# Kernel optimization log

Hardware: AMD Instinct MI355X
Metric: run time of the kernel (lower is better)

Reference implementation:

```python
import jax, jax.numpy as jnp
import numpy as np

EMBED_DIM = 1024
N_HEADS = 16
HEAD_DIM = EMBED_DIM // N_HEADS
BATCH = 2
SEQ = 2048


def setup_inputs() -> dict:
    key = jax.random.key(0)
    ks = jax.random.split(key, 12)
    s = 1.0 / np.sqrt(EMBED_DIM)
    return {
        "x": jax.random.normal(ks[0], (BATCH, SEQ, EMBED_DIM), jnp.float32),
        "q_w": jax.random.normal(ks[1], (EMBED_DIM, EMBED_DIM), jnp.float32) * s,
        "q_b": jax.random.normal(ks[2], (EMBED_DIM,), jnp.float32) * s,
        "k_w": jax.random.normal(ks[3], (EMBED_DIM, EMBED_DIM), jnp.float32) * s,
        "k_b": jax.random.normal(ks[4], (EMBED_DIM,), jnp.float32) * s,
        "v_w": jax.random.normal(ks[5], (EMBED_DIM, EMBED_DIM), jnp.float32) * s,
        "v_b": jax.random.normal(ks[6], (EMBED_DIM,), jnp.float32) * s,
        "phase": jax.random.normal(ks[7], (N_HEADS, HEAD_DIM), jnp.float32),
        "entanglement": jax.random.normal(ks[8], (N_HEADS, HEAD_DIM, HEAD_DIM), jnp.float32) * 0.1,
        "out_w": jax.random.normal(ks[9], (EMBED_DIM, EMBED_DIM), jnp.float32) * s,
        "out_b": jax.random.normal(ks[10], (EMBED_DIM,), jnp.float32) * s,
    }


def reference(x, q_w, q_b, k_w, k_b, v_w, v_b, phase, entanglement, out_w, out_b):
    b, s, _ = x.shape
    # projections -> [b, h, s, d]
    def split_heads(y):
        return y.reshape(b, s, N_HEADS, HEAD_DIM).transpose(0, 2, 1, 3)
    Q = split_heads(x @ q_w + q_b)
    K = split_heads(x @ k_w + k_b)
    V = split_heads(x @ v_w + v_b)
    # real part of phase-rotated Q/K: Q * cos(phase) (imag discarded by .real)
    cosp = jnp.cos(phase)[None, :, None, :]  # [1, h, 1, d]
    Qc = Q * cosp
    Kc = K * cosp
    scores = jnp.einsum('bhqd,bhkd->bhqk', Qc, Kc) / np.sqrt(HEAD_DIM)
    # bilinear entanglement term: Q . E . K^T per head
    scores = scores + jnp.einsum('bhqd,hde,bhke->bhqk', Q, entanglement, K)
    attn = jax.nn.softmax(scores, axis=-1)
    attended = jnp.einsum('bhqk,bhkd->bhqd', attn, V)
    attended = attended.transpose(0, 2, 1, 3).reshape(b, s, EMBED_DIM)
    return attended @ out_w + out_b
```

## Files before the change

### kernel.cpp

```cpp
#include <hip/hip_runtime.h>
#include <hip/hip_bf16.h>

typedef __bf16 bf16;
typedef __bf16 bf16x8 __attribute__((ext_vector_type(8)));
typedef __bf16 bf16x4 __attribute__((ext_vector_type(4)));
typedef float f32x4 __attribute__((ext_vector_type(4)));
typedef float f32x16 __attribute__((ext_vector_type(16)));
typedef unsigned int u32x2 __attribute__((ext_vector_type(2)));

#define EMBED 1024
#define NH 16
#define HD 64
#define BATCH 2
#define SEQ 2048
#define MTOK 4096
#define LOG2E 1.4426950408889634f

static __device__ __forceinline__ float fast_exp2(float x) {
#if __has_builtin(__builtin_amdgcn_exp2f)
  return __builtin_amdgcn_exp2f(x);
#else
  float r;
  asm("v_exp_f32 %0, %1" : "=v"(r) : "v"(x));
  return r;
#endif
}

static __device__ __forceinline__ f32x4 mfma16(bf16x8 a, bf16x8 b, f32x4 c) {
  return __builtin_amdgcn_mfma_f32_16x16x32_bf16(a, b, c, 0, 0, 0);
}
static __device__ __forceinline__ f32x16 mfma32(bf16x8 a, bf16x8 b, f32x16 c) {
  return __builtin_amdgcn_mfma_f32_32x32x16_bf16(a, b, c, 0, 0, 0);
}

static __device__ __forceinline__ void gld_lds16(const bf16* g, bf16* l) {
  __builtin_amdgcn_global_load_lds(
      (const __attribute__((address_space(1))) void*)g,
      (__attribute__((address_space(3))) void*)l, 16, 0, 0);
}

__global__ __launch_bounds__(256) void prep_kernel(
    const float* __restrict__ x, const float* __restrict__ qw,
    const float* __restrict__ qb, const float* __restrict__ kw,
    const float* __restrict__ vw, const float* __restrict__ ow,
    const float* __restrict__ ent, const float* __restrict__ phase,
    bf16* __restrict__ xb, bf16* __restrict__ wtall, bf16* __restrict__ wot,
    float* __restrict__ beff) {
  __shared__ float t0[64][65];
  __shared__ float t1[64][65];
  const int bb = blockIdx.x;
  const int tid = threadIdx.x;

  if (bb < 2048) {
    const int n4 = MTOK * EMBED / 4;
    int i = bb * 256 + tid;
    for (; i < n4; i += 2048 * 256) {
      f32x4 v = ((const f32x4*)x)[i];
      bf16x4 o;
      o[0] = (bf16)v[0]; o[1] = (bf16)v[1]; o[2] = (bf16)v[2]; o[3] = (bf16)v[3];
      ((bf16x4*)xb)[i] = o;
    }
    return;
  }
  if (bb < 2816) {
    const int idx = (bb - 2048) & 255;
    const float* W = (bb < 2304) ? kw : (bb < 2560) ? vw : ow;
    bf16* Wt = (bb < 2304) ? (wtall + 1024 * 1024)
             : (bb < 2560) ? (wtall + 2 * 1024 * 1024) : wot;
    const int bc = (idx & 15) * 64;
    const int br = (idx >> 4) * 64;
#pragma unroll
    for (int j = 0; j < 16; j++) {
      int id2 = j * 256 + tid;
      int r = id2 >> 6, c = id2 & 63;
      t0[r][c] = W[(size_t)(br + r) * EMBED + bc + c];
    }
    __syncthreads();
#pragma unroll
    for (int j = 0; j < 16; j++) {
      int id2 = j * 256 + tid;
      int r = id2 >> 6, c = id2 & 63;
      Wt[(size_t)(bc + r) * EMBED + br + c] = (bf16)t0[c][r];
    }
    return;
  }
  if (bb < 3072) {
    const int idx = bb - 2816;
    const int h = idx >> 4;
    const int ibase = (idx & 15) * 64;
#pragma unroll
    for (int j = 0; j < 16; j++) {
      int id2 = j * 256 + tid;
      int i = id2 >> 6, d = id2 & 63;
      t0[i][d] = qw[(size_t)(ibase + i) * EMBED + h * HD + d];
    }
#pragma unroll
    for (int j = 0; j < 16; j++) {
      int id2 = j * 256 + tid;
      int d = id2 >> 6, e = id2 & 63;
      float v = ent[((size_t)h * HD + d) * HD + e];
      if (d == e) { float cp = cosf(phase[h * HD + d]); v += cp * cp * 0.125f; }
      t1[d][e] = v * LOG2E;
    }
    __syncthreads();
    const int i = tid & 63;
    const int e0 = (tid >> 6) * 16;
    float s[16];
#pragma unroll
    for (int ee = 0; ee < 16; ee++) s[ee] = 0.f;
    for (int d = 0; d < 64; d++) {
      float qv = t0[i][d];
#pragma unroll
      for (int ee = 0; ee < 16; ee++) s[ee] += qv * t1[d][e0 + ee];
    }
#pragma unroll
    for (int ee = 0; ee < 16; ee++)
      wtall[(size_t)(h * HD + e0 + ee) * EMBED + ibase + i] = (bf16)s[ee];
    return;
  }
  const int h = bb - 3072;
  if (tid < 64) {
    const int e = tid;
    float s = 0.f;
    for (int d = 0; d < 64; d++) {
      float v = ent[((size_t)h * HD + d) * HD + e];
      if (d == e) { float cp = cosf(phase[h * HD + d]); v += cp * cp * 0.125f; }
      s += qb[h * HD + d] * v;
    }
    beff[h * HD + e] = s * LOG2E;
  }
}

template <int EPI>
__global__ __launch_bounds__(256) void gemm_bt_kernel(
    const bf16* __restrict__ A, const bf16* __restrict__ Bt,
    const float* __restrict__ bias_q, const float* __restrict__ bias_k,
    const float* __restrict__ bias_v, const float* __restrict__ bias_o,
    bf16* __restrict__ Qp, bf16* __restrict__ Kp, bf16* __restrict__ Vt,
    float* __restrict__ Fout) {
  const int tid = threadIdx.x;
  const int lane = tid & 63, w = tid >> 6;
  const int g = lane >> 4, r15 = lane & 15;
  const int wr = w >> 1, wc = w & 1;
  const int bm = blockIdx.x * 128;
  const int bn = blockIdx.y * 128;

  __shared__ bf16 sA[128 * 32];
  __shared__ bf16 sB[128 * 32];

  f32x4 acc[4][4];
#pragma unroll
  for (int m = 0; m < 4; m++)
#pragma unroll
    for (int n = 0; n < 4; n++) acc[m][n] = (f32x4){0.f, 0.f, 0.f, 0.f};

  const int srow = tid >> 2;
  const int scol = (tid & 3) << 3;
  const bf16* aptr = A + (size_t)(bm + srow) * EMBED + scol;
  const bf16* bptr = Bt + (size_t)(bn + srow) * EMBED + scol;
  bf16* la = sA + tid * 8;
  bf16* lb = sB + tid * 8;

  for (int k0 = 0; k0 < EMBED; k0 += 32) {
    __syncthreads();
    gld_lds16(aptr + k0, la);
    gld_lds16(aptr + k0 + 64 * EMBED, la + 64 * 32);
    gld_lds16(bptr + k0, lb);
    gld_lds16(bptr + k0 + 64 * EMBED, lb + 64 * 32);
    __syncthreads();
    bf16x8 af[4], bfv[4];
#pragma unroll
    for (int m = 0; m < 4; m++)
      af[m] = *(const bf16x8*)&sA[(wr * 64 + m * 16 + r15) * 32 + g * 8];
#pragma unroll
    for (int n = 0; n < 4; n++)
      bfv[n] = *(const bf16x8*)&sB[(wc * 64 + n * 16 + r15) * 32 + g * 8];
#pragma unroll
    for (int m = 0; m < 4; m++)
#pragma unroll
      for (int n = 0; n < 4; n++) acc[m][n] = mfma16(af[m], bfv[n], acc[m][n]);
  }

  const int orow0 = bm + wr * 64;
  if (EPI == 0) {
    const int seg = bn >> 10;
    const int clb = (bn & 1023) + wc * 64;
#pragma unroll
    for (int n = 0; n < 4; n++) {
      const int cl = clb + n * 16 + r15;
      const float bias = (seg == 0) ? bias_q[cl] : (seg == 1) ? bias_k[cl] : bias_v[cl];
#pragma unroll
      for (int m = 0; m < 4; m++) {
        const int row0 = orow0 + m * 16 + g * 4;
        if (seg == 2) {
          const int b = row0 >> 11, s = row0 & 2047;
          const int hh = cl >> 6, d = cl & 63;
          bf16x4 pk;
#pragma unroll
          for (int r = 0; r < 4; r++) pk[r] = (bf16)(acc[m][n][r] + bias);
          *(bf16x4*)(Vt + ((size_t)((b * NH + hh) * HD + d)) * SEQ + s) = pk;
        } else {
          bf16* dst = ((seg == 0) ? Qp : Kp) + (size_t)row0 * EMBED + cl;
#pragma unroll
          for (int r = 0; r < 4; r++) dst[(size_t)r * EMBED] = (bf16)(acc[m][n][r] + bias);
        }
      }
    }
  } else {
    const int ocol0 = bn + wc * 64;
#pragma unroll
    for (int n = 0; n < 4; n++) {
      const int col = ocol0 + n * 16 + r15;
      const float bias = bias_o[col];
#pragma unroll
      for (int m = 0; m < 4; m++) {
        const int row0 = orow0 + m * 16 + g * 4;
#pragma unroll
        for (int r = 0; r < 4; r++)
          Fout[(size_t)(row0 + r) * EMBED + col] = acc[m][n][r] + bias;
      }
    }
  }
}

__global__ __launch_bounds__(256, 3) void flash_attn_kernel(
    const bf16* __restrict__ Qp, const bf16* __restrict__ Kp,
    const bf16* __restrict__ Vt, bf16* __restrict__ Op) {
  const int tid = threadIdx.x, lane = tid & 63, w = tid >> 6;
  const int q31 = lane & 31, hi = lane >> 5;
  const int flat = blockIdx.x;
  const int c = (flat & 7) * 64 + (flat >> 3);
  const int bh = c >> 4, qt = c & 15;
  const int b = bh >> 4, h = bh & 15;

  __shared__ bf16 sK[2][4096];
  __shared__ bf16 sV[2][4096];

  const int strow = tid >> 3;
  const int stcolb = (tid & 7) << 4;
  const int stsb = stcolb ^ ((strow & 7) << 4);

  const char* kgbase = (const char*)(Kp + ((size_t)b * SEQ) * EMBED + h * HD);
  const char* vgbase = (const char*)(Vt + (size_t)bh * HD * SEQ);

  auto stage = [&](int buf, int kv0) {
#pragma unroll
    for (int i = 0; i < 2; i++) {
      const int row = i * 32 + strow;
      gld_lds16((const bf16*)(kgbase + (size_t)(kv0 + row) * (EMBED * 2) + stsb),
                &sK[buf][i * 2048 + tid * 8]);
    }
#pragma unroll
    for (int i = 0; i < 2; i++) {
      const int row = i * 32 + strow;
      gld_lds16((const bf16*)(vgbase + (size_t)row * (SEQ * 2) + (size_t)kv0 * 2 + stsb),
                &sV[buf][i * 2048 + tid * 8]);
    }
  };

  stage(0, 0);

  const int qbase = qt * 128 + w * 32;
  const int qrow = qbase + q31;
  const bf16* qptr = Qp + ((size_t)(b * SEQ + qrow)) * EMBED + h * HD;
  bf16x8 aq[4];
#pragma unroll
  for (int ds = 0; ds < 4; ds++)
    aq[ds] = *(const bf16x8*)(qptr + ds * 16 + hi * 8);

  const int sz = (q31 & 7) << 4;
  int cofs[4];
#pragma unroll
  for (int i = 0; i < 4; i++) cofs[i] = ((i * 32 + hi * 16) ^ sz);

  f32x16 o0, o1;
#pragma unroll
  for (int i = 0; i < 16; i++) { o0[i] = 0.f; o1[i] = 0.f; }
  float mrow = -3.0e38f, lrow = 0.f;

  for (int it = 0; it < SEQ / 64; ++it) {
    const int cur = it & 1;
    if (it + 1 < SEQ / 64) {
      stage(cur ^ 1, (it + 1) * 64);
      asm volatile("s_waitcnt vmcnt(4)" ::: "memory");
    } else {
      asm volatile("s_waitcnt vmcnt(0)" ::: "memory");
    }
    __builtin_amdgcn_s_barrier();

    const char* kc = (const char*)&sK[cur][0] + q31 * 128;
    const char* vc = (const char*)&sV[cur][0] + q31 * 128;

    f32x16 s0, s1;
#pragma unroll
    for (int i = 0; i < 16; i++) { s0[i] = 0.f; s1[i] = 0.f; }
    __builtin_amdgcn_s_setprio(1);
#pragma unroll
    for (int ds = 0; ds < 4; ds++) {
      bf16x8 bk0 = *(const bf16x8*)(kc + cofs[ds]);
      bf16x8 bk1 = *(const bf16x8*)(kc + 4096 + cofs[ds]);
      s0 = mfma32(bk0, aq[ds], s0);
      s1 = mfma32(bk1, aq[ds], s1);
    }
    __builtin_amdgcn_s_setprio(0);

    float mt = s0[0];
#pragma unroll
    for (int i = 1; i < 16; i++) mt = fmaxf(mt, s0[i]);
#pragma unroll
    for (int i = 0; i < 16; i++) mt = fmaxf(mt, s1[i]);
    {
      u32x2 sm = __builtin_amdgcn_permlane32_swap(__float_as_uint(mt),
                                                  __float_as_uint(mt), false, false);
      mt = fmaxf(__uint_as_float(sm.x), __uint_as_float(sm.y));
    }
    if (__any(mt > mrow + 8.f)) {
      const float mn = fmaxf(mrow, mt);
      const float al = fast_exp2(mrow - mn);
      mrow = mn;
      lrow *= al;
      o0 *= al;
      o1 *= al;
    }

    union B4 { bf16x4 v; unsigned int u[2]; };
    B4 qd[8];
    float lsum = 0.f;
#pragma unroll
    for (int j = 0; j < 4; j++)
#pragma unroll
      for (int r = 0; r < 4; r++) {
        float pv = fast_exp2(s0[4 * j + r] - mrow);
        lsum += pv;
        qd[j].v[r] = (bf16)pv;
      }
#pragma unroll
    for (int j = 0; j < 4; j++)
#pragma unroll
      for (int r = 0; r < 4; r++) {
        float pv = fast_exp2(s1[4 * j + r] - mrow);
        lsum += pv;
        qd[4 + j].v[r] = (bf16)pv;
      }
    {
      u32x2 ss = __builtin_amdgcn_permlane32_swap(__float_as_uint(lsum),
                                                  __float_as_uint(lsum), false, false);
      lrow += __uint_as_float(ss.x) + __uint_as_float(ss.y);
    }

    bf16x8 pfrag[4];
#pragma unroll
    for (int kt = 0; kt < 4; kt++) {
      u32x2 p0 = __builtin_amdgcn_permlane32_swap(qd[2 * kt].u[0],
                                                  qd[2 * kt + 1].u[0], false, false);
      u32x2 p1 = __builtin_amdgcn_permlane32_swap(qd[2 * kt].u[1],
                                                  qd[2 * kt + 1].u[1], false, false);
      union { unsigned int u[4]; bf16x8 v; } f;
      f.u[0] = p0.x; f.u[1] = p1.x; f.u[2] = p0.y; f.u[3] = p1.y;
      pfrag[kt] = f.v;
    }

    __builtin_amdgcn_s_setprio(1);
#pragma unroll
    for (int kt = 0; kt < 4; kt++) {
      bf16x8 av0 = *(const bf16x8*)(vc + cofs[kt]);
      bf16x8 av1 = *(const bf16x8*)(vc + 4096 + cofs[kt]);
      o0 = mfma32(av0, pfrag[kt], o0);
      o1 = mfma32(av1, pfrag[kt], o1);
    }
    __builtin_amdgcn_s_setprio(0);
    __builtin_amdgcn_s_barrier();
  }

  const float inv = 1.f / lrow;
  bf16* obase = Op + ((size_t)(b * SEQ + qrow)) * EMBED + h * HD;
#pragma unroll
  for (int j = 0; j < 4; j++) {
    bf16x4 st;
#pragma unroll
    for (int r = 0; r < 4; r++) st[r] = (bf16)(o0[4 * j + r] * inv);
    *(bf16x4*)(obase + 8 * j + 4 * hi) = st;
  }
#pragma unroll
  for (int j = 0; j < 4; j++) {
    bf16x4 st;
#pragma unroll
    for (int r = 0; r < 4; r++) st[r] = (bf16)(o1[4 * j + r] * inv);
    *(bf16x4*)(obase + 32 + 8 * j + 4 * hi) = st;
  }
}

extern "C" void kernel_launch(void* const* d_in, const int* in_sizes, int n_in,
                              void* d_out, int out_size, void* d_ws, size_t ws_size,
                              hipStream_t stream) {
  const float* x     = (const float*)d_in[0];
  const float* q_w   = (const float*)d_in[1];
  const float* q_b   = (const float*)d_in[2];
  const float* k_w   = (const float*)d_in[3];
  const float* k_b   = (const float*)d_in[4];
  const float* v_w   = (const float*)d_in[5];
  const float* v_b   = (const float*)d_in[6];
  const float* phase = (const float*)d_in[7];
  const float* ent   = (const float*)d_in[8];
  const float* out_w = (const float*)d_in[9];
  const float* out_b = (const float*)d_in[10];
  float* out = (float*)d_out;

  char* ws = (char*)d_ws;
  bf16* xb    = (bf16*)(ws + 0);
  bf16* wtall = (bf16*)(ws + 8388608);
  bf16* wot   = (bf16*)(ws + 14680064);
  float* beff = (float*)(ws + 16777216);
  bf16* Qp    = (bf16*)(ws + 16781312);
  bf16* Kp    = (bf16*)(ws + 25169920);
  bf16* Vt    = (bf16*)(ws + 33558528);
  (void)in_sizes; (void)n_in; (void)out_size; (void)ws_size;

  prep_kernel<<<3088, 256, 0, stream>>>(x, q_w, q_b, k_w, v_w, out_w, ent, phase,
                                        xb, wtall, wot, beff);

  gemm_bt_kernel<0><<<dim3(32, 24), 256, 0, stream>>>(
      xb, wtall, beff, k_b, v_b, nullptr, Qp, Kp, Vt, nullptr);

  flash_attn_kernel<<<512, 256, 0, stream>>>(Qp, Kp, Vt, xb);

  gemm_bt_kernel<1><<<dim3(32, 8), 256, 0, stream>>>(
      xb, wot, nullptr, nullptr, nullptr, out_b, nullptr, nullptr, nullptr, out);
}
```

Measured before the change: 140.6 us.

## Split attention KV sequence across two wave groups and merge softmax partials

Flash attention blocks grow to 512 threads. Each half of the block processes half of the KV sequence with its own double-buffered LDS tiles, and the two partial softmax states are merged through shared memory at the end. This doubles the waves per query tile to raise occupancy and latency hiding on the 512-block grid, since 512 blocks of 4 waves underfill the GPU. The cost is 64KB of LDS per block, which limits blocks per CU, plus an extra sync and merge step.

```diff
diff --git a/kernel.cpp b/kernel.cpp
--- a/kernel.cpp
+++ b/kernel.cpp
@@ -223,44 +223,46 @@
   }
 }
 
-__global__ __launch_bounds__(256, 3) void flash_attn_kernel(
+__global__ __launch_bounds__(512, 4) void flash_attn_kernel(
     const bf16* __restrict__ Qp, const bf16* __restrict__ Kp,
     const bf16* __restrict__ Vt, bf16* __restrict__ Op) {
   const int tid = threadIdx.x, lane = tid & 63, w = tid >> 6;
   const int q31 = lane & 31, hi = lane >> 5;
+  const int half = w >> 2, wq = w & 3;
   const int flat = blockIdx.x;
   const int c = (flat & 7) * 64 + (flat >> 3);
   const int bh = c >> 4, qt = c & 15;
   const int b = bh >> 4, h = bh & 15;
 
-  __shared__ bf16 sK[2][4096];
-  __shared__ bf16 sV[2][4096];
-
-  const int strow = tid >> 3;
-  const int stcolb = (tid & 7) << 4;
-  const int stsb = stcolb ^ ((strow & 7) << 4);
+  __shared__ char smem[65536];
+  bf16* sKb = (bf16*)smem;
+  bf16* sVb = (bf16*)(smem + 32768);
+
+  const int g256 = tid & 255;
+  const int strow = g256 >> 3;
+  const int stcb = (g256 & 7) << 4;
 
   const char* kgbase = (const char*)(Kp + ((size_t)b * SEQ) * EMBED + h * HD);
   const char* vgbase = (const char*)(Vt + (size_t)bh * HD * SEQ);
 
   auto stage = [&](int buf, int kv0) {
+    bf16* kd = sKb + (size_t)(half * 2 + buf) * 4096 + g256 * 8;
+    bf16* vd = sVb + (size_t)(half * 2 + buf) * 4096 + g256 * 8;
 #pragma unroll
     for (int i = 0; i < 2; i++) {
       const int row = i * 32 + strow;
-      gld_lds16((const bf16*)(kgbase + (size_t)(kv0 + row) * (EMBED * 2) + stsb),
-                &sK[buf][i * 2048 + tid * 8]);
-    }
-#pragma unroll
-    for (int i = 0; i < 2; i++) {
-      const int row = i * 32 + strow;
-      gld_lds16((const bf16*)(vgbase + (size_t)row * (SEQ * 2) + (size_t)kv0 * 2 + stsb),
-                &sV[buf][i * 2048 + tid * 8]);
+      const int sb = stcb ^ ((row & 7) << 4);
+      gld_lds16((const bf16*)(kgbase + (size_t)(kv0 + row) * (EMBED * 2) + sb),
+                kd + i * 2048);
+      gld_lds16((const bf16*)(vgbase + (size_t)row * (SEQ * 2) + (size_t)kv0 * 2 + sb),
+                vd + i * 2048);
     }
   };
 
-  stage(0, 0);
-
-  const int qbase = qt * 128 + w * 32;
+  const int kvbase = half * 1024;
+  stage(0, kvbase);
+
+  const int qbase = qt * 128 + wq * 32;
   const int qrow = qbase + q31;
   const bf16* qptr = Qp + ((size_t)(b * SEQ + qrow)) * EMBED + h * HD;
   bf16x8 aq[4];
@@ -278,18 +280,20 @@
   for (int i = 0; i < 16; i++) { o0[i] = 0.f; o1[i] = 0.f; }
   float mrow = -3.0e38f, lrow = 0.f;
 
-  for (int it = 0; it < SEQ / 64; ++it) {
+  union B4 { bf16x4 v; unsigned int u[2]; };
+
+  for (int it = 0; it < 16; ++it) {
     const int cur = it & 1;
-    if (it + 1 < SEQ / 64) {
-      stage(cur ^ 1, (it + 1) * 64);
+    if (it + 1 < 16) {
+      stage(cur ^ 1, kvbase + (it + 1) * 64);
       asm volatile("s_waitcnt vmcnt(4)" ::: "memory");
     } else {
       asm volatile("s_waitcnt vmcnt(0)" ::: "memory");
     }
     __builtin_amdgcn_s_barrier();
 
-    const char* kc = (const char*)&sK[cur][0] + q31 * 128;
-    const char* vc = (const char*)&sV[cur][0] + q31 * 128;
+    const char* kc = (const char*)(sKb + (size_t)(half * 2 + cur) * 4096) + q31 * 128;
+    const char* vc = (const char*)(sVb + (size_t)(half * 2 + cur) * 4096) + q31 * 128;
 
     f32x16 s0, s1;
 #pragma unroll
@@ -323,7 +327,6 @@
       o1 *= al;
     }
 
-    union B4 { bf16x4 v; unsigned int u[2]; };
     B4 qd[8];
     float lsum = 0.f;
 #pragma unroll
@@ -372,21 +375,42 @@
     __builtin_amdgcn_s_barrier();
   }
 
-  const float inv = 1.f / lrow;
-  bf16* obase = Op + ((size_t)(b * SEQ + qrow)) * EMBED + h * HD;
-#pragma unroll
-  for (int j = 0; j < 4; j++) {
-    bf16x4 st;
-#pragma unroll
-    for (int r = 0; r < 4; r++) st[r] = (bf16)(o0[4 * j + r] * inv);
-    *(bf16x4*)(obase + 8 * j + 4 * hi) = st;
-  }
-#pragma unroll
-  for (int j = 0; j < 4; j++) {
-    bf16x4 st;
-#pragma unroll
-    for (int r = 0; r < 4; r++) st[r] = (bf16)(o1[4 * j + r] * inv);
-    *(bf16x4*)(obase + 32 + 8 * j + 4 * hi) = st;
+  float* shO = (float*)smem;
+  float* shML = (float*)(smem + 33792);
+  if (half == 1) {
+    float* o = shO + (size_t)(wq * 64 + lane) * 33;
+#pragma unroll
+    for (int i = 0; i < 16; i++) { o[i] = o0[i]; o[16 + i] = o1[i]; }
+    shML[(wq * 64 + lane) * 2] = mrow;
+    shML[(wq * 64 + lane) * 2 + 1] = lrow;
+  }
+  __syncthreads();
+  if (half == 0) {
+    const float* o = shO + (size_t)(wq * 64 + lane) * 33;
+    const float mB = shML[(wq * 64 + lane) * 2];
+    const float lB = shML[(wq * 64 + lane) * 2 + 1];
+    const float M = fmaxf(mrow, mB);
+    const float wA = fast_exp2(mrow - M), wB = fast_exp2(mB - M);
+    const float inv = 1.f / (lrow * wA + lB * wB);
+    const float fA = wA * inv, fB = wB * inv;
+
+    bf16* obase = Op + ((size_t)(b * SEQ + qrow)) * EMBED + h * HD;
+#pragma unroll
+    for (int j = 0; j < 4; j++) {
+      bf16x4 st;
+#pragma unroll
+      for (int r = 0; r < 4; r++)
+        st[r] = (bf16)(o0[4 * j + r] * fA + o[4 * j + r] * fB);
+      *(bf16x4*)(obase + 8 * j + 4 * hi) = st;
+    }
+#pragma unroll
+    for (int j = 0; j < 4; j++) {
+      bf16x4 st;
+#pragma unroll
+      for (int r = 0; r < 4; r++)
+        st[r] = (bf16)(o1[4 * j + r] * fA + o[16 + 4 * j + r] * fB);
+      *(bf16x4*)(obase + 32 + 8 * j + 4 * hi) = st;
+    }
   }
 }
 
@@ -422,7 +446,7 @@
   gemm_bt_kernel<0><<<dim3(32, 24), 256, 0, stream>>>(
       xb, wtall, beff, k_b, v_b, nullptr, Qp, Kp, Vt, nullptr);
 
-  flash_attn_kernel<<<512, 256, 0, stream>>>(Qp, Kp, Vt, xb);
+  flash_attn_kernel<<<512, 512, 0, stream>>>(Qp, Kp, Vt, xb);
 
   gemm_bt_kernel<1><<<dim3(32, 8), 256, 0, stream>>>(
       xb, wot, nullptr, nullptr, nullptr, out_b, nullptr, nullptr, nullptr, out);
```

Result: faster. 137.4 us (-2.2%).
